# Kernel tuning notes

Hardware: AMD Instinct MI355X
Metric: run time of the kernel (lower is better)

## Reference

```python
import jax, jax.numpy as jnp
import numpy as np
import math

D_MODEL = 128
N_HEAD = 8
D_K = D_MODEL // N_HEAD
NEG_INF = -1e30


def setup_inputs() -> dict:
    key = jax.random.key(0)
    ks = jax.random.split(key, 8)
    B, N, D = 4, 2048, D_MODEL
    s = 1.0 / math.sqrt(D)
    x = jax.random.normal(ks[0], (B, D, N), dtype=jnp.float32)
    mask = jnp.ones((B, N), dtype=jnp.float32)
    Wq = jax.random.normal(ks[1], (D, D), dtype=jnp.float32) * s
    Wk = jax.random.normal(ks[2], (D, D), dtype=jnp.float32) * s
    Wv = jax.random.normal(ks[3], (D, D), dtype=jnp.float32) * s
    Wfc = jax.random.normal(ks[4], (D, D), dtype=jnp.float32) * s
    z = jnp.zeros((D,), dtype=jnp.float32)
    return {"x": x, "mask": mask, "Wq": Wq, "bq": z, "Wk": Wk, "bk": z,
            "Wv": Wv, "bv": z, "Wfc": Wfc, "bfc": z}


def reference(x, mask, Wq, bq, Wk, bk, Wv, bv, Wfc, bfc):
    # x: [B, D, N], mask: [B, N]
    B, D, N = x.shape
    xt = jnp.swapaxes(x, 1, 2)  # [B, N, D]
    q = (xt @ Wq.T + bq).reshape(B, N, N_HEAD, D_K)
    k = (xt @ Wk.T + bk).reshape(B, N, N_HEAD, D_K)
    v = (xt @ Wv.T + bv).reshape(B, N, N_HEAD, D_K)
    # scores: [B, H, Nq, Nk]; NOTE: original scales by sqrt(d_model), not sqrt(d_k)
    scores = jnp.einsum('bnhd,bmhd->bhnm', q, k) / jnp.sqrt(jnp.float32(D))
    # multiplicative mask_logits over the key dimension
    m = mask[:, None, None, :]  # [B, 1, 1, Nk]
    scores = scores * m + (1.0 - m) * NEG_INF
    atten = jax.nn.softmax(scores, axis=-1)  # dropout is identity (p=0 / eval)
    out = jnp.einsum('bhnm,bmhd->bnhd', atten, v).reshape(B, N, D)
    out = out @ Wfc.T + bfc
    return jnp.swapaxes(out, 1, 2)  # [B, D, N]
```

## Files before the change

kernel.cpp:

```cpp
#include <hip/hip_runtime.h>
#include <stdint.h>

#define BSZ  4
#define NSEQ 2048
#define DM   128
#define NH   8
#define DK   16
#define LOG2E 1.4426950408889634f
#define SCALE_QL 0.1275156338341935f
#define W_SCALE 3.814697265625e-6f

typedef __bf16          bf16x8v __attribute__((ext_vector_type(8)));
typedef float           f32x4   __attribute__((ext_vector_type(4)));
typedef float           f32x16  __attribute__((ext_vector_type(16)));
typedef unsigned short  u16x8   __attribute__((ext_vector_type(8)));
typedef unsigned short  u16x4   __attribute__((ext_vector_type(4)));
typedef unsigned int    u32x2   __attribute__((ext_vector_type(2)));
typedef unsigned int    u32x4   __attribute__((ext_vector_type(4)));

__device__ __forceinline__ unsigned short f2bf(float f) {
    unsigned u = __float_as_uint(f);
    u = (u + 0x7fffu + ((u >> 16) & 1u)) >> 16;
    return (unsigned short)u;
}

__device__ __forceinline__ unsigned int pack2bf(float a, float b) {
#if __has_builtin(__builtin_amdgcn_cvt_pk_bf16_f32)
    typedef __bf16 bf16x2 __attribute__((ext_vector_type(2)));
    bf16x2 v = __builtin_amdgcn_cvt_pk_bf16_f32(a, b);
    return __builtin_bit_cast(unsigned int, v);
#else
    return (unsigned)f2bf(a) | ((unsigned)f2bf(b) << 16);
#endif
}

__device__ __forceinline__ float exp2_(float x) {
#if __has_builtin(__builtin_amdgcn_exp2f)
    return __builtin_amdgcn_exp2f(x);
#else
    return exp2f(x);
#endif
}

__device__ __forceinline__ u16x8 cvt8(const float* p, float sc) {
    const f32x4 a = *reinterpret_cast<const f32x4*>(p);
    const f32x4 b = *reinterpret_cast<const f32x4*>(p + 4);
    u32x4 u = {pack2bf(a[0] * sc, a[1] * sc), pack2bf(a[2] * sc, a[3] * sc),
               pack2bf(b[0] * sc, b[1] * sc), pack2bf(b[2] * sc, b[3] * sc)};
    return __builtin_bit_cast(u16x8, u);
}

__device__ __forceinline__ f32x4 mfma16(u16x8 a, u16x8 b, f32x4 c) {
    return __builtin_amdgcn_mfma_f32_16x16x32_bf16(
        __builtin_bit_cast(bf16x8v, a), __builtin_bit_cast(bf16x8v, b), c, 0, 0, 0);
}
__device__ __forceinline__ f32x16 mfma32(u16x8 a, u16x8 b, f32x16 c) {
    return __builtin_amdgcn_mfma_f32_32x32x16_bf16(
        __builtin_bit_cast(bf16x8v, a), __builtin_bit_cast(bf16x8v, b), c, 0, 0, 0);
}

__global__ __launch_bounds__(768) void k_qkv(
    const float* __restrict__ x,
    const float* __restrict__ Wq, const float* __restrict__ bq,
    const float* __restrict__ Wk, const float* __restrict__ bk,
    const float* __restrict__ Wv, const float* __restrict__ bv,
    const float* __restrict__ Wfc, const float* __restrict__ mask,
    unsigned short* __restrict__ Q, unsigned short* __restrict__ Kb,
    unsigned short* __restrict__ Vt,
    unsigned short* __restrict__ WfcB, unsigned short* __restrict__ wb)
{
    __shared__ __align__(16) float xs[DM * 36];
    const int tid = threadIdx.x;

    const int gt = blockIdx.x * 768 + tid;
    if (gt < DM * DM) {
        WfcB[gt] = f2bf(Wfc[gt]);
    } else if (gt < DM * DM + BSZ * NSEQ) {
        const int i = gt - DM * DM;
        wb[i] = f2bf(mask[i] * W_SCALE);
    }

    const int b  = blockIdx.x >> 6;
    const int n0 = (blockIdx.x & 63) << 5;

#pragma unroll
    for (int i = tid; i < 1024; i += 768) {
        const int d = i >> 3, c4 = (i & 7) << 2;
        *reinterpret_cast<f32x4*>(&xs[d * 36 + c4]) =
            *reinterpret_cast<const f32x4*>(x + (size_t)(b * DM + d) * NSEQ + n0 + c4);
    }
    __syncthreads();

    const int lane = tid & 63;
    const int wv   = tid >> 6;
    const int mat  = wv >> 2;
    const int nt   = (wv >> 1) & 1;
    const int th   = wv & 1;
    const int c    = lane & 15;
    const int quad = lane >> 4;
    const int col  = n0 + nt * 16 + c;

    u16x8 xf[4];
#pragma unroll
    for (int kk = 0; kk < 4; ++kk) {
        float f[8];
#pragma unroll
        for (int j = 0; j < 8; ++j)
            f[j] = xs[(kk * 32 + quad * 8 + j) * 36 + nt * 16 + c];
        u32x4 u = {pack2bf(f[0], f[1]), pack2bf(f[2], f[3]),
                   pack2bf(f[4], f[5]), pack2bf(f[6], f[7])};
        xf[kk] = __builtin_bit_cast(u16x8, u);
    }

    const float* W    = (mat == 0) ? Wq : (mat == 1) ? Wk : Wv;
    const float* bias = (mat == 0) ? bq : (mat == 1) ? bk : bv;
    const float  sc   = (mat == 0) ? SCALE_QL : 1.0f;
    const float  vw   = (mat == 2) ? mask[b * NSEQ + col] * W_SCALE : 0.f;

#pragma unroll
    for (int tt = 0; tt < 4; ++tt) {
        const int t = th * 4 + tt;
        f32x4 acc = {0.f, 0.f, 0.f, 0.f};
#pragma unroll
        for (int kk = 0; kk < 4; ++kk)
            acc = mfma16(cvt8(W + (t * 16 + c) * DM + kk * 32 + quad * 8, sc),
                         xf[kk], acc);
        if (mat == 2) {
#pragma unroll
            for (int r = 0; r < 4; ++r)
                Vt[((b * NH + t) * DK + quad * 4 + r) * NSEQ + col] =
                    f2bf((acc[r] + bias[t * 16 + quad * 4 + r]) * vw);
        } else {
            u16x4 pk;
#pragma unroll
            for (int r = 0; r < 4; ++r)
                pk[r] = f2bf(acc[r] + bias[t * 16 + quad * 4 + r] * sc);
            *reinterpret_cast<u16x4*>(
                (mat == 0 ? Q : Kb) + ((size_t)(b * NH + t) * NSEQ + col) * DK +
                quad * 4) = pk;
        }
    }
}

__global__ __launch_bounds__(256, 6) void k_attn(
    const unsigned short* __restrict__ Q,
    const unsigned short* __restrict__ Kb,
    const unsigned short* __restrict__ Vt,
    const unsigned short* __restrict__ wb,
    unsigned short* __restrict__ AO)
{
    __shared__ __align__(16) char smem[17408];
    const int tid  = threadIdx.x;
    const int lane = tid & 63;
    const int w    = tid >> 6;
    const int q32  = lane & 31;
    const int c    = lane & 15;
    const int quad = lane >> 4;
    const int hi   = lane >> 5;

    const int bid = ((int)blockIdx.x & 7) * 256 + ((int)blockIdx.x >> 3);
    const int b  = bid >> 9;
    const int h  = (bid >> 6) & 7;
    const int n0 = (bid & 63) << 5;
    const int bh = b * NH + h;

    const u16x8 uq = *reinterpret_cast<const u16x8*>(
        Q + ((size_t)bh * NSEQ + n0 + q32) * DK + 8 * hi);

    const unsigned short* Kp = Kb + (size_t)bh * NSEQ * DK + 8 * hi;
    const unsigned short* Vp = Vt + ((size_t)bh * DK + c) * NSEQ + 8 * quad;
    const unsigned short* wp = wb + b * NSEQ + 8 * quad;

    char* pb = smem + w * 4352;
    char* wrow = pb + q32 * 136 + 8 * hi;
    const char* rrow0 = pb + c * 136 + 16 * quad;
    const char* rrow1 = pb + (c + 16) * 136 + 16 * quad;

    f32x4 o0 = {0.f, 0.f, 0.f, 0.f}, o1 = {0.f, 0.f, 0.f, 0.f};
    f32x4 l0 = {0.f, 0.f, 0.f, 0.f}, l1 = {0.f, 0.f, 0.f, 0.f};
    const f32x16 z16 = {};
    const int kvb = w * (NSEQ / 4);

    u16x8 nk0 = *reinterpret_cast<const u16x8*>(Kp + (size_t)(kvb + q32) * DK);
    u16x8 nk1 = *reinterpret_cast<const u16x8*>(Kp + (size_t)(kvb + 32 + q32) * DK);

#pragma unroll 1
    for (int it = 0; it < 8; ++it) {
        const int kv0 = kvb + it * 64;

        const u16x8 uv0 = *reinterpret_cast<const u16x8*>(Vp + kv0);
        const u16x8 uv1 = *reinterpret_cast<const u16x8*>(Vp + kv0 + 32);

        {
            __builtin_amdgcn_s_setprio(1);
            f32x16 S0 = mfma32(nk0, uq, z16);
            __builtin_amdgcn_s_setprio(0);
            if (it < 7)
                nk0 = *reinterpret_cast<const u16x8*>(
                    Kp + (size_t)(kv0 + 64 + q32) * DK);
#pragma unroll
            for (int i = 0; i < 16; ++i) S0[i] = exp2_(S0[i]);
#pragma unroll
            for (int g = 0; g < 4; ++g) {
                u32x2 d = {pack2bf(S0[4 * g], S0[4 * g + 1]),
                           pack2bf(S0[4 * g + 2], S0[4 * g + 3])};
                *reinterpret_cast<u32x2*>(wrow + 16 * g) = d;
            }
        }

        {
            __builtin_amdgcn_s_setprio(1);
            f32x16 S1 = mfma32(nk1, uq, z16);
            __builtin_amdgcn_s_setprio(0);
            if (it < 7)
                nk1 = *reinterpret_cast<const u16x8*>(
                    Kp + (size_t)(kv0 + 96 + q32) * DK);
#pragma unroll
            for (int i = 0; i < 16; ++i) S1[i] = exp2_(S1[i]);
#pragma unroll
            for (int g = 0; g < 4; ++g) {
                u32x2 d = {pack2bf(S1[4 * g], S1[4 * g + 1]),
                           pack2bf(S1[4 * g + 2], S1[4 * g + 3])};
                *reinterpret_cast<u32x2*>(wrow + 64 + 16 * g) = d;
            }
        }

        const u16x8 up0a = *reinterpret_cast<const u16x8*>(rrow0);
        const u16x8 up1a = *reinterpret_cast<const u16x8*>(rrow1);
        const u16x8 up0b = *reinterpret_cast<const u16x8*>(rrow0 + 64);
        const u16x8 up1b = *reinterpret_cast<const u16x8*>(rrow1 + 64);
        const u16x8 uw0 = *reinterpret_cast<const u16x8*>(wp + kv0);
        const u16x8 uw1 = *reinterpret_cast<const u16x8*>(wp + kv0 + 32);

        __builtin_amdgcn_s_setprio(1);
        o0 = mfma16(uv0, up0a, o0);
        o1 = mfma16(uv0, up1a, o1);
        l0 = mfma16(uw0, up0a, l0);
        l1 = mfma16(uw0, up1a, l1);
        o0 = mfma16(uv1, up0b, o0);
        o1 = mfma16(uv1, up1b, o1);
        l0 = mfma16(uw1, up0b, l0);
        l1 = mfma16(uw1, up1b, l1);
        __builtin_amdgcn_s_setprio(0);
    }

    __syncthreads();
    float* Lsm = reinterpret_cast<float*>(smem);
    float* Osm = reinterpret_cast<float*>(smem + 512);
    Lsm[w * 32 + c]      = l0[0];
    Lsm[w * 32 + 16 + c] = l1[0];
    *reinterpret_cast<f32x4*>(Osm + w * 640 + c * 20 + 4 * quad)        = o0;
    *reinterpret_cast<f32x4*>(Osm + w * 640 + (c + 16) * 20 + 4 * quad) = o1;
    __syncthreads();

    const int q   = tid >> 3;
    const int dk2 = (tid & 7) * 2;
    const float l = Lsm[q] + Lsm[32 + q] + Lsm[64 + q] + Lsm[96 + q];
    const float* Oq = Osm + q * 20 + dk2;
    const float v0 = Oq[0] + Oq[640] + Oq[1280] + Oq[1920];
    const float v1 = Oq[1] + Oq[641] + Oq[1281] + Oq[1921];
    const float inv = 1.0f / l;
    *reinterpret_cast<unsigned int*>(
        AO + ((size_t)(b * NSEQ) + n0 + q) * DM + h * DK + dk2) =
        pack2bf(v0 * inv, v1 * inv);
}

__global__ __launch_bounds__(256) void k_fc(
    const unsigned short* __restrict__ AO,
    const unsigned short* __restrict__ WfcB, const float* __restrict__ bfc,
    float* __restrict__ out)
{
    const int lane = threadIdx.x & 63;
    const int w    = threadIdx.x >> 6;
    const int c    = lane & 15;
    const int quad = lane >> 4;
    const int b    = blockIdx.x >> 8;
    const int n0   = ((blockIdx.x >> 1) & 127) << 4;
    const int t    = (blockIdx.x & 1) * 4 + w;

    u16x8 af[4];
#pragma unroll
    for (int kk = 0; kk < 4; ++kk)
        af[kk] = *reinterpret_cast<const u16x8*>(
            AO + ((size_t)(b * NSEQ) + n0 + c) * DM + kk * 32 + quad * 8);

    f32x4 acc = {0.f, 0.f, 0.f, 0.f};
#pragma unroll
    for (int kk = 0; kk < 4; ++kk)
        acc = mfma16(*reinterpret_cast<const u16x8*>(
                         WfcB + (t * 16 + c) * DM + kk * 32 + quad * 8),
                     af[kk], acc);
#pragma unroll
    for (int r = 0; r < 4; ++r)
        out[(size_t)(b * DM + t * 16 + quad * 4 + r) * NSEQ + n0 + c] =
            acc[r] + bfc[t * 16 + quad * 4 + r];
}

extern "C" void kernel_launch(void* const* d_in, const int* in_sizes, int n_in,
                              void* d_out, int out_size, void* d_ws, size_t ws_size,
                              hipStream_t stream)
{
    const float* x    = (const float*)d_in[0];
    const float* mask = (const float*)d_in[1];
    const float* Wq   = (const float*)d_in[2];
    const float* bq   = (const float*)d_in[3];
    const float* Wk   = (const float*)d_in[4];
    const float* bk   = (const float*)d_in[5];
    const float* Wv   = (const float*)d_in[6];
    const float* bv   = (const float*)d_in[7];
    const float* Wfc  = (const float*)d_in[8];
    const float* bfc  = (const float*)d_in[9];
    float* out = (float*)d_out;

    const size_t QKV_ELEMS = (size_t)BSZ * NH * NSEQ * DK;
    unsigned short* Q    = (unsigned short*)d_ws;
    unsigned short* Kb   = Q + QKV_ELEMS;
    unsigned short* Vt   = Kb + QKV_ELEMS;
    unsigned short* AO   = Vt + QKV_ELEMS;
    unsigned short* WfcB = AO + QKV_ELEMS;
    unsigned short* wb   = WfcB + DM * DM;

    k_qkv<<<256, 768, 0, stream>>>(x, Wq, bq, Wk, bk, Wv, bv, Wfc, mask,
                                   Q, Kb, Vt, WfcB, wb);
    k_attn<<<2048, 256, 0, stream>>>(Q, Kb, Vt, wb, AO);
    k_fc<<<1024, 256, 0, stream>>>(AO, WfcB, bfc, out);
}
```

Measured before the change: 130.1 us.

## Keep P in registers via bpermute and fuse V and mask-weight into one 32x32 MFMA

```diff
diff --git a/kernel.cpp b/kernel.cpp
--- a/kernel.cpp
+++ b/kernel.cpp
@@ -59,6 +59,15 @@
         __builtin_bit_cast(bf16x8v, a), __builtin_bit_cast(bf16x8v, b), c, 0, 0, 0);
 }
 
+__device__ __forceinline__ void xpair(unsigned lo, unsigned hi_, int bpi, int isHi,
+                                      unsigned& wA, unsigned& wB) {
+    const unsigned send = isHi ? lo : hi_;
+    const unsigned recv =
+        (unsigned)__builtin_amdgcn_ds_bpermute(bpi, (int)send);
+    wA = isHi ? recv : lo;
+    wB = isHi ? hi_ : recv;
+}
+
 __global__ __launch_bounds__(768) void k_qkv(
     const float* __restrict__ x,
     const float* __restrict__ Wq, const float* __restrict__ bq,
@@ -66,8 +75,7 @@
     const float* __restrict__ Wv, const float* __restrict__ bv,
     const float* __restrict__ Wfc, const float* __restrict__ mask,
     unsigned short* __restrict__ Q, unsigned short* __restrict__ Kb,
-    unsigned short* __restrict__ Vt,
-    unsigned short* __restrict__ WfcB, unsigned short* __restrict__ wb)
+    unsigned short* __restrict__ VW2, unsigned short* __restrict__ WfcB)
 {
     __shared__ __align__(16) float xs[DM * 36];
     const int tid = threadIdx.x;
@@ -76,8 +84,16 @@
     if (gt < DM * DM) {
         WfcB[gt] = f2bf(Wfc[gt]);
     } else if (gt < DM * DM + BSZ * NSEQ) {
-        const int i = gt - DM * DM;
-        wb[i] = f2bf(mask[i] * W_SCALE);
+        const int i  = gt - DM * DM;
+        const int kv = i & (NSEQ - 1);
+        const int bb = i >> 11;
+        const unsigned short w16 = f2bf(mask[i] * W_SCALE);
+        unsigned short* dst = VW2 +
+            (((size_t)(bb * NH) * 128 + (kv >> 4)) << 9) +
+            (16 + ((kv >> 3) & 1) * 32) * 8 + (kv & 7);
+#pragma unroll
+        for (int hh = 0; hh < NH; ++hh)
+            dst[(size_t)hh * 128 * 512] = w16;
     }
 
     const int b  = blockIdx.x >> 6;
@@ -115,7 +131,10 @@
     const float* W    = (mat == 0) ? Wq : (mat == 1) ? Wk : Wv;
     const float* bias = (mat == 0) ? bq : (mat == 1) ? bk : bv;
     const float  sc   = (mat == 0) ? SCALE_QL : 1.0f;
-    const float  vw   = (mat == 2) ? mask[b * NSEQ + col] * W_SCALE : 0.f;
+    const float  vwsc = (mat == 2) ? mask[b * NSEQ + col] * W_SCALE : 0.f;
+    const int    g    = col >> 4;
+    const int    roff = ((col >> 3) & 1) * 32;
+    const int    j7   = col & 7;
 
 #pragma unroll
     for (int tt = 0; tt < 4; ++tt) {
@@ -126,10 +145,12 @@
             acc = mfma16(cvt8(W + (t * 16 + c) * DM + kk * 32 + quad * 8, sc),
                          xf[kk], acc);
         if (mat == 2) {
+            unsigned short* vwp = VW2 +
+                (((size_t)((b * NH + t) * 128 + g)) << 9) + j7;
 #pragma unroll
             for (int r = 0; r < 4; ++r)
-                Vt[((b * NH + t) * DK + quad * 4 + r) * NSEQ + col] =
-                    f2bf((acc[r] + bias[t * 16 + quad * 4 + r]) * vw);
+                vwp[(quad * 4 + r + roff) * 8] =
+                    f2bf((acc[r] + bias[t * 16 + quad * 4 + r]) * vwsc);
         } else {
             u16x4 pk;
 #pragma unroll
@@ -142,21 +163,19 @@
     }
 }
 
-__global__ __launch_bounds__(256, 6) void k_attn(
+__global__ __launch_bounds__(256, 4) void k_attn(
     const unsigned short* __restrict__ Q,
     const unsigned short* __restrict__ Kb,
-    const unsigned short* __restrict__ Vt,
-    const unsigned short* __restrict__ wb,
+    const unsigned short* __restrict__ VW2,
     unsigned short* __restrict__ AO)
 {
-    __shared__ __align__(16) char smem[17408];
+    __shared__ __align__(16) float smem[128 + 4 * 32 * 20];
     const int tid  = threadIdx.x;
     const int lane = tid & 63;
     const int w    = tid >> 6;
     const int q32  = lane & 31;
-    const int c    = lane & 15;
-    const int quad = lane >> 4;
     const int hi   = lane >> 5;
+    const int bpi  = (lane ^ 32) << 2;
 
     const int bid = ((int)blockIdx.x & 7) * 256 + ((int)blockIdx.x >> 3);
     const int b  = bid >> 9;
@@ -168,16 +187,9 @@
         Q + ((size_t)bh * NSEQ + n0 + q32) * DK + 8 * hi);
 
     const unsigned short* Kp = Kb + (size_t)bh * NSEQ * DK + 8 * hi;
-    const unsigned short* Vp = Vt + ((size_t)bh * DK + c) * NSEQ + 8 * quad;
-    const unsigned short* wp = wb + b * NSEQ + 8 * quad;
-
-    char* pb = smem + w * 4352;
-    char* wrow = pb + q32 * 136 + 8 * hi;
-    const char* rrow0 = pb + c * 136 + 16 * quad;
-    const char* rrow1 = pb + (c + 16) * 136 + 16 * quad;
-
-    f32x4 o0 = {0.f, 0.f, 0.f, 0.f}, o1 = {0.f, 0.f, 0.f, 0.f};
-    f32x4 l0 = {0.f, 0.f, 0.f, 0.f}, l1 = {0.f, 0.f, 0.f, 0.f};
+    const unsigned short* Ap = VW2 + (((size_t)bh * 128) << 9) + lane * 8;
+
+    f32x16 acc = {};
     const f32x16 z16 = {};
     const int kvb = w * (NSEQ / 4);
 
@@ -187,70 +199,79 @@
 #pragma unroll 1
     for (int it = 0; it < 8; ++it) {
         const int kv0 = kvb + it * 64;
-
-        const u16x8 uv0 = *reinterpret_cast<const u16x8*>(Vp + kv0);
-        const u16x8 uv1 = *reinterpret_cast<const u16x8*>(Vp + kv0 + 32);
-
+        const int g0  = kv0 >> 4;
+        const u16x8 va0 = *reinterpret_cast<const u16x8*>(Ap + ((size_t)(g0    ) << 9));
+        const u16x8 va1 = *reinterpret_cast<const u16x8*>(Ap + ((size_t)(g0 + 1) << 9));
+        const u16x8 va2 = *reinterpret_cast<const u16x8*>(Ap + ((size_t)(g0 + 2) << 9));
+        const u16x8 va3 = *reinterpret_cast<const u16x8*>(Ap + ((size_t)(g0 + 3) << 9));
+
+        u16x8 bf1, bf2;
         {
             __builtin_amdgcn_s_setprio(1);
-            f32x16 S0 = mfma32(nk0, uq, z16);
+            f32x16 S = mfma32(nk0, uq, z16);
             __builtin_amdgcn_s_setprio(0);
             if (it < 7)
                 nk0 = *reinterpret_cast<const u16x8*>(
                     Kp + (size_t)(kv0 + 64 + q32) * DK);
 #pragma unroll
-            for (int i = 0; i < 16; ++i) S0[i] = exp2_(S0[i]);
-#pragma unroll
-            for (int g = 0; g < 4; ++g) {
-                u32x2 d = {pack2bf(S0[4 * g], S0[4 * g + 1]),
-                           pack2bf(S0[4 * g + 2], S0[4 * g + 3])};
-                *reinterpret_cast<u32x2*>(wrow + 16 * g) = d;
-            }
+            for (int i = 0; i < 16; ++i) S[i] = exp2_(S[i]);
+            const unsigned a0 = pack2bf(S[0],  S[1]),  a1 = pack2bf(S[2],  S[3]);
+            const unsigned b0 = pack2bf(S[4],  S[5]),  b1 = pack2bf(S[6],  S[7]);
+            const unsigned c0 = pack2bf(S[8],  S[9]),  c1 = pack2bf(S[10], S[11]);
+            const unsigned d0 = pack2bf(S[12], S[13]), d1 = pack2bf(S[14], S[15]);
+            unsigned w0, w1, w2, w3, y0, y1, y2, y3;
+            xpair(a0, b0, bpi, hi, w0, w2);
+            xpair(a1, b1, bpi, hi, w1, w3);
+            xpair(c0, d0, bpi, hi, y0, y2);
+            xpair(c1, d1, bpi, hi, y1, y3);
+            const u32x4 f1 = {w0, w1, w2, w3};
+            const u32x4 f2 = {y0, y1, y2, y3};
+            bf1 = __builtin_bit_cast(u16x8, f1);
+            bf2 = __builtin_bit_cast(u16x8, f2);
         }
-
+        __builtin_amdgcn_s_setprio(1);
+        acc = mfma32(va0, bf1, acc);
+        acc = mfma32(va1, bf2, acc);
+        __builtin_amdgcn_s_setprio(0);
+
+        u16x8 bf3, bf4;
         {
             __builtin_amdgcn_s_setprio(1);
-            f32x16 S1 = mfma32(nk1, uq, z16);
+            f32x16 S = mfma32(nk1, uq, z16);
             __builtin_amdgcn_s_setprio(0);
             if (it < 7)
                 nk1 = *reinterpret_cast<const u16x8*>(
                     Kp + (size_t)(kv0 + 96 + q32) * DK);
 #pragma unroll
-            for (int i = 0; i < 16; ++i) S1[i] = exp2_(S1[i]);
-#pragma unroll
-            for (int g = 0; g < 4; ++g) {
-                u32x2 d = {pack2bf(S1[4 * g], S1[4 * g + 1]),
-                           pack2bf(S1[4 * g + 2], S1[4 * g + 3])};
-                *reinterpret_cast<u32x2*>(wrow + 64 + 16 * g) = d;
-            }
+            for (int i = 0; i < 16; ++i) S[i] = exp2_(S[i]);
+            const unsigned a0 = pack2bf(S[0],  S[1]),  a1 = pack2bf(S[2],  S[3]);
+            const unsigned b0 = pack2bf(S[4],  S[5]),  b1 = pack2bf(S[6],  S[7]);
+            const unsigned c0 = pack2bf(S[8],  S[9]),  c1 = pack2bf(S[10], S[11]);
+            const unsigned d0 = pack2bf(S[12], S[13]), d1 = pack2bf(S[14], S[15]);
+            unsigned w0, w1, w2, w3, y0, y1, y2, y3;
+            xpair(a0, b0, bpi, hi, w0, w2);
+            xpair(a1, b1, bpi, hi, w1, w3);
+            xpair(c0, d0, bpi, hi, y0, y2);
+            xpair(c1, d1, bpi, hi, y1, y3);
+            const u32x4 f3 = {w0, w1, w2, w3};
+            const u32x4 f4 = {y0, y1, y2, y3};
+            bf3 = __builtin_bit_cast(u16x8, f3);
+            bf4 = __builtin_bit_cast(u16x8, f4);
         }
-
-        const u16x8 up0a = *reinterpret_cast<const u16x8*>(rrow0);
-        const u16x8 up1a = *reinterpret_cast<const u16x8*>(rrow1);
-        const u16x8 up0b = *reinterpret_cast<const u16x8*>(rrow0 + 64);
-        const u16x8 up1b = *reinterpret_cast<const u16x8*>(rrow1 + 64);
-        const u16x8 uw0 = *reinterpret_cast<const u16x8*>(wp + kv0);
-        const u16x8 uw1 = *reinterpret_cast<const u16x8*>(wp + kv0 + 32);
-
         __builtin_amdgcn_s_setprio(1);
-        o0 = mfma16(uv0, up0a, o0);
-        o1 = mfma16(uv0, up1a, o1);
-        l0 = mfma16(uw0, up0a, l0);
-        l1 = mfma16(uw0, up1a, l1);
-        o0 = mfma16(uv1, up0b, o0);
-        o1 = mfma16(uv1, up1b, o1);
-        l0 = mfma16(uw1, up0b, l0);
-        l1 = mfma16(uw1, up1b, l1);
+        acc = mfma32(va2, bf3, acc);
+        acc = mfma32(va3, bf4, acc);
         __builtin_amdgcn_s_setprio(0);
     }
 
-    __syncthreads();
-    float* Lsm = reinterpret_cast<float*>(smem);
-    float* Osm = reinterpret_cast<float*>(smem + 512);
-    Lsm[w * 32 + c]      = l0[0];
-    Lsm[w * 32 + 16 + c] = l1[0];
-    *reinterpret_cast<f32x4*>(Osm + w * 640 + c * 20 + 4 * quad)        = o0;
-    *reinterpret_cast<f32x4*>(Osm + w * 640 + (c + 16) * 20 + 4 * quad) = o1;
+    float* Lsm = smem;
+    float* Osm = smem + 128;
+    float* Orow = Osm + w * 640 + q32 * 20;
+    *reinterpret_cast<f32x4*>(Orow + (hi ? 4 : 0)) =
+        f32x4{acc[0], acc[1], acc[2], acc[3]};
+    *reinterpret_cast<f32x4*>(Orow + (hi ? 12 : 8)) =
+        f32x4{acc[4], acc[5], acc[6], acc[7]};
+    if (!hi) Lsm[w * 32 + q32] = acc[8];
     __syncthreads();
 
     const int q   = tid >> 3;
@@ -315,13 +336,12 @@
     const size_t QKV_ELEMS = (size_t)BSZ * NH * NSEQ * DK;
     unsigned short* Q    = (unsigned short*)d_ws;
     unsigned short* Kb   = Q + QKV_ELEMS;
-    unsigned short* Vt   = Kb + QKV_ELEMS;
-    unsigned short* AO   = Vt + QKV_ELEMS;
+    unsigned short* AO   = Kb + QKV_ELEMS;
     unsigned short* WfcB = AO + QKV_ELEMS;
-    unsigned short* wb   = WfcB + DM * DM;
+    unsigned short* VW2  = WfcB + DM * DM;
 
     k_qkv<<<256, 768, 0, stream>>>(x, Wq, bq, Wk, bk, Wv, bv, Wfc, mask,
-                                   Q, Kb, Vt, WfcB, wb);
-    k_attn<<<2048, 256, 0, stream>>>(Q, Kb, Vt, wb, AO);
+                                   Q, Kb, VW2, WfcB);
+    k_attn<<<2048, 256, 0, stream>>>(Q, Kb, VW2, AO);
     k_fc<<<1024, 256, 0, stream>>>(AO, WfcB, bfc, out);
 }
```

New measurement: 122.4 us. 5.9% less time.
